# Kernel tuning notes

Hardware: AMD Instinct MI355X
Metric: run time of the kernel (lower is better)

The kernel has to match this reference:

```python
import jax, jax.numpy as jnp
import numpy as np

LN_EPS = 1e-6

def _log_g(x):
    return jnp.where(x >= 0, jnp.log(jax.nn.relu(x) + 0.5), -jax.nn.softplus(-x))

def setup_inputs() -> dict:
    key = jax.random.key(0)
    k1, k2 = jax.random.split(key)
    B, T, D = 8, 4096, 1024
    x = jax.random.normal(k1, (B, T, D), dtype=jnp.float32)
    W = jax.random.normal(k2, (D, 2 * D), dtype=jnp.float32) * (1.0 / np.sqrt(D))
    b = jnp.zeros((2 * D,), dtype=jnp.float32)
    gamma = jnp.ones((D,), dtype=jnp.float32)
    beta = jnp.zeros((D,), dtype=jnp.float32)
    return {"x": x, "W": W, "b": b, "gamma": gamma, "beta": beta}

def reference(x, W, b, gamma, beta):
    # projection: [B,T,D] @ [D,2D] -> [B,T,2D]
    projected = jnp.einsum('btd,de->bte', x, W) + b
    h_tilde, k = jnp.split(projected, 2, axis=-1)
    log_coeffs = -jax.nn.softplus(k)          # log(1-z)
    log_z = -jax.nn.softplus(-k)               # log(z)
    log_values = log_z + _log_g(h_tilde)
    # parallel scan in log space along time axis (-2)
    a_star = jnp.cumsum(log_coeffs, axis=-2)
    log_h0_plus_b_star = jax.lax.associative_scan(jnp.logaddexp, log_values - a_star, axis=-2)
    h = jnp.exp(a_star + log_h0_plus_b_star)
    # residual + LayerNorm (eps = flax nnx default 1e-6)
    y = x + h
    mu = jnp.mean(y, axis=-1, keepdims=True)
    var = jnp.mean(jnp.square(y - mu), axis=-1, keepdims=True)
    return (y - mu) * jax.lax.rsqrt(var + LN_EPS) * gamma + beta
```

## Files before the change

kernel.cpp:

```cpp
#include <hip/hip_runtime.h>
#include <hip/hip_bf16.h>

#define B_  8
#define T_  4096
#define D_  1024
#define M_  (B_*T_)
#define N_  (2*D_)
#define K_  D_
#define NC_ 32
#define C_  (T_/NC_)

typedef short bf16x8 __attribute__((ext_vector_type(8)));
typedef float f32x4  __attribute__((ext_vector_type(4)));

__device__ __forceinline__ unsigned short f2bf(float f) {
  union { float f; unsigned int u; } v; v.f = f;
  unsigned int r = (v.u + 0x7fffu + ((v.u >> 16) & 1u)) >> 16;
  return (unsigned short)r;
}

__device__ __forceinline__ float bf2f(unsigned short u) {
  union { unsigned int u; float f; } v; v.u = ((unsigned int)u) << 16; return v.f;
}

__device__ __forceinline__ float sigm(float x) {
  return 1.0f / (1.0f + __expf(-x));
}

__device__ __forceinline__ void async16(const void* g, void* l) {
  __builtin_amdgcn_global_load_lds((const __attribute__((address_space(1))) void*)g,
                                   (__attribute__((address_space(3))) void*)l,
                                   16, 0, 0);
}

__global__ void cast_x_kernel(const float* __restrict__ x, unsigned short* __restrict__ xb) {
  const long n4 = (long)M_ * K_ / 4;
  long i = (long)blockIdx.x * blockDim.x + threadIdx.x;
  const long stride = (long)gridDim.x * blockDim.x;
  for (; i < n4; i += stride) {
    float4 v = ((const float4*)x)[i];
    ushort4 o;
    o.x = f2bf(v.x); o.y = f2bf(v.y); o.z = f2bf(v.z); o.w = f2bf(v.w);
    ((ushort4*)xb)[i] = o;
  }
}

__global__ void cast_wt_kernel(const float* __restrict__ W, unsigned short* __restrict__ Wt) {
  __shared__ float tile[32][33];
  const int n0 = blockIdx.x * 32, k0 = blockIdx.y * 32;
  const int tx = threadIdx.x, ty = threadIdx.y;
  for (int i = 0; i < 32; i += 8)
    tile[ty + i][tx] = W[(size_t)(k0 + ty + i) * N_ + n0 + tx];
  __syncthreads();
  for (int i = 0; i < 32; i += 8)
    Wt[(size_t)(n0 + ty + i) * K_ + k0 + tx] = f2bf(tile[tx][ty + i]);
}

#define BM 256
#define BN 256
#define BK 64
#define NT (K_/BK)
#define LDSA(b) ((b)*32768)
#define LDSB(b) ((b)*32768 + 16384)

#define BARX()  __builtin_amdgcn_s_barrier()
#define LGKM0() asm volatile("s_waitcnt lgkmcnt(0)" ::: "memory")
#define SB0()   __builtin_amdgcn_sched_barrier(0)
#define VM8()   asm volatile("s_waitcnt vmcnt(8)" ::: "memory")
#define VM0()   asm volatile("s_waitcnt vmcnt(0)" ::: "memory")

#define STAGE_Bt(BUF, KOFF) do {                                                \
    _Pragma("unroll")                                                           \
    for (int r = 0; r < 4; ++r)                                                 \
      async16(aB + (KOFF) + r*64*K_, lds + LDSB(BUF) + w*512 + r*4096);         \
  } while (0)
#define STAGE_At(BUF, KOFF) do {                                                \
    _Pragma("unroll")                                                           \
    for (int r = 0; r < 4; ++r)                                                 \
      async16(aA + (KOFF) + r*64*K_, lds + LDSA(BUF) + w*512 + r*4096);         \
  } while (0)

#define RD_A(MBASE, BUF) do {                                                   \
    _Pragma("unroll")                                                           \
    for (int m = 0; m < 4; ++m) {                                               \
      af[m][0] = *(const bf16x8*)(lds + LDSA(BUF) + (rowA + (MBASE + m)*16)*64 + cc0); \
      af[m][1] = *(const bf16x8*)(lds + LDSA(BUF) + (rowA + (MBASE + m)*16)*64 + cc1); \
    } } while (0)
#define RD_B(NBASE, BUF) do {                                                   \
    _Pragma("unroll")                                                           \
    for (int n = 0; n < 2; ++n) {                                               \
      bfr[NBASE + n][0] = *(const bf16x8*)(lds + LDSB(BUF) + (rowB + (NBASE + n)*16)*64 + cc0); \
      bfr[NBASE + n][1] = *(const bf16x8*)(lds + LDSB(BUF) + (rowB + (NBASE + n)*16)*64 + cc1); \
    } } while (0)

#define MFMA_Q(MB, NB) do {                                                     \
    __builtin_amdgcn_s_setprio(1);                                              \
    _Pragma("unroll")                                                           \
    for (int m = 0; m < 4; ++m)                                                 \
      _Pragma("unroll")                                                         \
      for (int n = 0; n < 2; ++n) {                                             \
        acc[MB+m][NB+n] = __builtin_amdgcn_mfma_f32_16x16x32_bf16(af[m][0], bfr[NB+n][0], acc[MB+m][NB+n], 0, 0, 0); \
        acc[MB+m][NB+n] = __builtin_amdgcn_mfma_f32_16x16x32_bf16(af[m][1], bfr[NB+n][1], acc[MB+m][NB+n], 0, 0, 0); \
      }                                                                         \
    __builtin_amdgcn_s_setprio(0);                                              \
  } while (0)

#define TILE(BUF, DO_STAGE, KOFF, VMW) do {                                     \
                                                                        \
    RD_A(0, BUF); RD_B(0, BUF);                                                 \
    BARX(); LGKM0(); SB0();                                                     \
    MFMA_Q(0, 0);                                                               \
    BARX();                                                                     \
                                                                        \
    RD_B(2, BUF);                                                               \
    BARX(); LGKM0(); SB0();                                                     \
    MFMA_Q(0, 2);                                                               \
    BARX();                                                                     \
                                                                        \
    if (DO_STAGE) STAGE_Bt(BUF, KOFF);                                          \
    RD_A(4, BUF);                                                               \
    BARX(); LGKM0(); SB0();                                                     \
    MFMA_Q(4, 0);                                                               \
    BARX();                                                                     \
                                                                        \
    if (DO_STAGE) STAGE_At(BUF, KOFF);                                          \
    MFMA_Q(4, 2);                                                               \
    VMW;                                                                        \
    BARX();                                                                     \
  } while (0)

__global__ __launch_bounds__(512, 2) void gemm_kernel(
    const unsigned short* __restrict__ A,
    const unsigned short* __restrict__ Bt,
    const float* __restrict__ bias,
    unsigned short* __restrict__ Sout,
    unsigned short* __restrict__ Gout) {
  __shared__ unsigned short lds[65536];

  const int tid  = threadIdx.x;
  const int w    = tid >> 6;
  const int lane = tid & 63;
  const int wm   = w >> 2;
  const int wn   = w & 3;
  const int quad = lane >> 4, n15 = lane & 15;

  const int bid   = blockIdx.x;
  const int xcd   = bid & 7;
  const int j     = bid >> 3;
  const int n_idx = j & 7;
  const int m_idx = (j >> 3) * 8 + xcd;
  const int m0 = m_idx * BM, n0 = n_idx * BN;

  const int lr = lane >> 3, lg = lane & 7;
  const int sg8 = (lg ^ lr) * 8;
  const unsigned short* aA = A  + (size_t)(m0 + w*8 + lr) * K_ + sg8;
  const unsigned short* aB = Bt + (size_t)(n0 + w*8 + lr) * K_ + sg8;

  const int n7  = n15 & 7;
  const int cc0 = (quad ^ n7) * 8;
  const int cc1 = cc0 ^ 32;
  const int rowA = wm * 128 + n15;
  const int rowB = wn * 64  + n15;

  f32x4 acc[8][4];
  #pragma unroll
  for (int i = 0; i < 8; ++i)
    #pragma unroll
    for (int jj = 0; jj < 4; ++jj) acc[i][jj] = (f32x4){0.f, 0.f, 0.f, 0.f};

  bf16x8 af[4][2], bfr[4][2];

  STAGE_Bt(0, 0);  STAGE_At(0, 0);
  STAGE_Bt(1, 64); STAGE_At(1, 64);
  VM8();
  BARX();

  int koff = 128;
  #pragma unroll 1
  for (int it = 0; it < 7; ++it) {
    TILE(0, 1, koff,      VM8());
    TILE(1, 1, koff + 64, VM8());
    koff += 128;
  }
  TILE(0, 0, 0, VM0());
  TILE(1, 0, 0, ((void)0));

  const bool is_k = (n0 >= D_);
  unsigned short* __restrict__ dst = is_k ? Sout : Gout;
  const int d0 = is_k ? (n0 - D_) : n0;
  float bv[4];
  #pragma unroll
  for (int jj = 0; jj < 4; ++jj) bv[jj] = bias[n0 + wn*64 + jj*16 + n15];

  #pragma unroll
  for (int i = 0; i < 8; ++i) {
    #pragma unroll
    for (int jj = 0; jj < 4; ++jj) {
      const int col = wn*64 + jj*16 + n15;
      #pragma unroll
      for (int r = 0; r < 4; ++r) {
        const int row = wm*128 + i*16 + quad*4 + r;
        const float val = acc[i][jj][r] + bv[jj];
        const float o = is_k ? sigm(val)
                             : ((val >= 0.0f) ? (val + 0.5f) : sigm(val));
        const int slot = (col >> 3) ^ (row & 7);
        lds[row*256 + slot*8 + (col & 7)] = f2bf(o);
      }
    }
  }
  __syncthreads();
  const int trow = tid >> 5;
  const int cg   = tid & 31;
  #pragma unroll
  for (int rr = 0; rr < 16; ++rr) {
    const int row = rr*16 + trow;
    const uint4 v = *(const uint4*)(lds + row*256 + ((cg ^ (row & 7)) * 8));
    *(uint4*)(dst + (size_t)(m0 + row) * D_ + d0 + cg*8) = v;
  }
}

__global__ void chunk_agg_kernel(const unsigned short* __restrict__ S,
                                 const unsigned short* __restrict__ G,
                                 float* __restrict__ AggA, float* __restrict__ AggV) {
  const int d = blockIdx.x * 256 + threadIdx.x;
  const int c = blockIdx.y;
  const int b = blockIdx.z;
  size_t base = ((size_t)b * T_ + (size_t)c * C_) * D_ + d;
  float Aa = 1.0f, V = 0.0f;
  for (int t = 0; t < C_; ++t) {
    const float s = bf2f(S[base]);
    const float g = bf2f(G[base]);
    const float a = 1.0f - s;
    V = fmaf(a, V, s * g);
    Aa *= a;
    base += D_;
  }
  const int idx = (b * NC_ + c) * D_ + d;
  AggA[idx] = Aa;
  AggV[idx] = V;
}

__global__ void chunk_scan_kernel(const float* __restrict__ AggA, const float* __restrict__ AggV,
                                  float* __restrict__ H0) {
  const int d = blockIdx.x * 256 + threadIdx.x;
  const int b = blockIdx.y;
  float h = 0.0f;
  for (int c = 0; c < NC_; ++c) {
    const int idx = (b * NC_ + c) * D_ + d;
    H0[idx] = h;
    h = fmaf(AggA[idx], h, AggV[idx]);
  }
}

__global__ __launch_bounds__(1024, 1) void scan_ln_kernel(
    const unsigned short* __restrict__ S, const unsigned short* __restrict__ G,
    const float* __restrict__ x, const float* __restrict__ H0,
    const float* __restrict__ gamma, const float* __restrict__ beta,
    float* __restrict__ out) {
  __shared__ float yb[16 * 1024];
  const int d = threadIdx.x;
  const int c = blockIdx.x;
  const int b = blockIdx.y;
  const int wid = d >> 6, lane = d & 63;

  float h = H0[(b * NC_ + c) * D_ + d];
  float gam[16], bet[16];
  for (int j = 0; j < 16; ++j) { gam[j] = gamma[lane + 64 * j]; bet[j] = beta[lane + 64 * j]; }

  size_t base = ((size_t)b * T_ + (size_t)c * C_) * D_ + d;
  for (int batch = 0; batch < 8; ++batch) {
    for (int tt = 0; tt < 16; ++tt) {
      const size_t idx = base + (size_t)tt * D_;
      const float s = bf2f(S[idx]);
      const float g = bf2f(G[idx]);
      h = fmaf(s, g - h, h);
      yb[tt * 1024 + d] = x[idx] + h;
    }
    __syncthreads();
    {
      float sy = 0.0f, sq = 0.0f;
      float yv[16];
      for (int j = 0; j < 16; ++j) {
        const float v = yb[wid * 1024 + lane + 64 * j];
        yv[j] = v; sy += v; sq += v * v;
      }
      for (int o = 32; o > 0; o >>= 1) {
        sy += __shfl_down(sy, o);
        sq += __shfl_down(sq, o);
      }
      sy = __shfl(sy, 0); sq = __shfl(sq, 0);
      const float mu   = sy * (1.0f / D_);
      const float rstd = rsqrtf(sq * (1.0f / D_) - mu * mu + 1e-6f);
      const size_t obase = ((size_t)b * T_ + (size_t)c * C_ + (size_t)batch * 16 + wid) * D_;
      for (int j = 0; j < 16; ++j)
        out[obase + lane + 64 * j] = (yv[j] - mu) * rstd * gam[j] + bet[j];
    }
    __syncthreads();
    base += (size_t)16 * D_;
  }
}

extern "C" void kernel_launch(void* const* d_in, const int* in_sizes, int n_in,
                              void* d_out, int out_size, void* d_ws, size_t ws_size,
                              hipStream_t stream) {
  const float* x     = (const float*)d_in[0];
  const float* W     = (const float*)d_in[1];
  const float* bias  = (const float*)d_in[2];
  const float* gamma = (const float*)d_in[3];
  const float* beta  = (const float*)d_in[4];
  float* out = (float*)d_out;

  char* ws = (char*)d_ws;
  unsigned short* Wt = (unsigned short*)ws;  ws += (size_t)N_ * K_ * 2;
  unsigned short* Xb = (unsigned short*)ws;  ws += (size_t)M_ * K_ * 2;
  unsigned short* S  = (unsigned short*)ws;  ws += (size_t)M_ * D_ * 2;
  unsigned short* G  = (unsigned short*)ws;  ws += (size_t)M_ * D_ * 2;
  float* AggA = (float*)ws;                  ws += (size_t)B_ * NC_ * D_ * 4;
  float* AggV = (float*)ws;                  ws += (size_t)B_ * NC_ * D_ * 4;
  float* H0   = (float*)ws;                  ws += (size_t)B_ * NC_ * D_ * 4;

  cast_x_kernel<<<4096, 256, 0, stream>>>(x, Xb);
  cast_wt_kernel<<<dim3(N_ / 32, K_ / 32), dim3(32, 8), 0, stream>>>(W, Wt);
  gemm_kernel<<<1024, 512, 0, stream>>>(Xb, Wt, bias, S, G);
  chunk_agg_kernel<<<dim3(D_ / 256, NC_, B_), 256, 0, stream>>>(S, G, AggA, AggV);
  chunk_scan_kernel<<<dim3(D_ / 256, B_), 256, 0, stream>>>(AggA, AggV, H0);
  scan_ln_kernel<<<dim3(NC_, B_), 1024, 0, stream>>>(S, G, x, H0, gamma, beta, out);
}
```

Measured before the change: 477.1 us.

## Restructure GEMM mainloop to single-stage prefetch with one barrier per K-tile

Replaces the two-tile-ahead pipeline, which used four barrier/lgkmcnt phases per K-tile, with a scheme that prefetches only the next K-tile into the other LDS buffer. Each tile is one block of LDS reads followed by MFMAs, ending with a full vmcnt(0) wait and __syncthreads. B fragments are split into two register arrays so all B reads happen up front, and A is read in two halves. The aim is to cut barrier and waitcnt overhead inside the loop. The cost is less latency hiding for global loads (one tile ahead instead of two) plus extra register pressure from holding all B fragments at once.

New measurement: 475.6 us. No clear change (-0.3%).

```diff
diff --git a/kernel.cpp b/kernel.cpp
--- a/kernel.cpp
+++ b/kernel.cpp
@@ -59,14 +59,10 @@
 #define BM 256
 #define BN 256
 #define BK 64
-#define NT (K_/BK)
 #define LDSA(b) ((b)*32768)
 #define LDSB(b) ((b)*32768 + 16384)
 
-#define BARX()  __builtin_amdgcn_s_barrier()
-#define LGKM0() asm volatile("s_waitcnt lgkmcnt(0)" ::: "memory")
 #define SB0()   __builtin_amdgcn_sched_barrier(0)
-#define VM8()   asm volatile("s_waitcnt vmcnt(8)" ::: "memory")
 #define VM0()   asm volatile("s_waitcnt vmcnt(0)" ::: "memory")
 
 #define STAGE_Bt(BUF, KOFF) do {                                                \
@@ -80,53 +76,43 @@
       async16(aA + (KOFF) + r*64*K_, lds + LDSA(BUF) + w*512 + r*4096);         \
   } while (0)
 
-#define RD_A(MBASE, BUF) do {                                                   \
+#define RD_A8(MBASE, BUF) do {                                                  \
     _Pragma("unroll")                                                           \
     for (int m = 0; m < 4; ++m) {                                               \
-      af[m][0] = *(const bf16x8*)(lds + LDSA(BUF) + (rowA + (MBASE + m)*16)*64 + cc0); \
-      af[m][1] = *(const bf16x8*)(lds + LDSA(BUF) + (rowA + (MBASE + m)*16)*64 + cc1); \
+      afA[m][0] = *(const bf16x8*)(lds + LDSA(BUF) + (rowA + (MBASE + m)*16)*64 + cc0); \
+      afA[m][1] = *(const bf16x8*)(lds + LDSA(BUF) + (rowA + (MBASE + m)*16)*64 + cc1); \
     } } while (0)
-#define RD_B(NBASE, BUF) do {                                                   \
+#define RD_B4(ARR, NBASE, BUF) do {                                             \
     _Pragma("unroll")                                                           \
     for (int n = 0; n < 2; ++n) {                                               \
-      bfr[NBASE + n][0] = *(const bf16x8*)(lds + LDSB(BUF) + (rowB + (NBASE + n)*16)*64 + cc0); \
-      bfr[NBASE + n][1] = *(const bf16x8*)(lds + LDSB(BUF) + (rowB + (NBASE + n)*16)*64 + cc1); \
+      ARR[n][0] = *(const bf16x8*)(lds + LDSB(BUF) + (rowB + (NBASE + n)*16)*64 + cc0); \
+      ARR[n][1] = *(const bf16x8*)(lds + LDSB(BUF) + (rowB + (NBASE + n)*16)*64 + cc1); \
     } } while (0)
 
-#define MFMA_Q(MB, NB) do {                                                     \
+#define MQ(BARR, MB, NB) do {                                                   \
     __builtin_amdgcn_s_setprio(1);                                              \
     _Pragma("unroll")                                                           \
     for (int m = 0; m < 4; ++m)                                                 \
       _Pragma("unroll")                                                         \
       for (int n = 0; n < 2; ++n) {                                             \
-        acc[MB+m][NB+n] = __builtin_amdgcn_mfma_f32_16x16x32_bf16(af[m][0], bfr[NB+n][0], acc[MB+m][NB+n], 0, 0, 0); \
-        acc[MB+m][NB+n] = __builtin_amdgcn_mfma_f32_16x16x32_bf16(af[m][1], bfr[NB+n][1], acc[MB+m][NB+n], 0, 0, 0); \
+        acc[MB+m][NB+n] = __builtin_amdgcn_mfma_f32_16x16x32_bf16(afA[m][0], BARR[n][0], acc[MB+m][NB+n], 0, 0, 0); \
+        acc[MB+m][NB+n] = __builtin_amdgcn_mfma_f32_16x16x32_bf16(afA[m][1], BARR[n][1], acc[MB+m][NB+n], 0, 0, 0); \
       }                                                                         \
     __builtin_amdgcn_s_setprio(0);                                              \
   } while (0)
 
-#define TILE(BUF, DO_STAGE, KOFF, VMW) do {                                     \
-                                                                        \
-    RD_A(0, BUF); RD_B(0, BUF);                                                 \
-    BARX(); LGKM0(); SB0();                                                     \
-    MFMA_Q(0, 0);                                                               \
-    BARX();                                                                     \
-                                                                        \
-    RD_B(2, BUF);                                                               \
-    BARX(); LGKM0(); SB0();                                                     \
-    MFMA_Q(0, 2);                                                               \
-    BARX();                                                                     \
-                                                                        \
-    if (DO_STAGE) STAGE_Bt(BUF, KOFF);                                          \
-    RD_A(4, BUF);                                                               \
-    BARX(); LGKM0(); SB0();                                                     \
-    MFMA_Q(4, 0);                                                               \
-    BARX();                                                                     \
-                                                                        \
-    if (DO_STAGE) STAGE_At(BUF, KOFF);                                          \
-    MFMA_Q(4, 2);                                                               \
-    VMW;                                                                        \
-    BARX();                                                                     \
+#define TILE_V2(BR, BW, DO_STAGE, KOFF) do {                                    \
+    RD_A8(0, BR);                                     \
+    RD_B4(bfrA, 0, BR);                               \
+    RD_B4(bfrB, 2, BR);                               \
+    if (DO_STAGE) { STAGE_Bt(BW, KOFF); STAGE_At(BW, KOFF); SB0(); }            \
+    MQ(bfrA, 0, 0);                                            \
+    MQ(bfrB, 0, 2);                                            \
+    RD_A8(4, BR);                                    \
+    MQ(bfrB, 4, 2);                                            \
+    MQ(bfrA, 4, 0);                                            \
+    VM0();                                                                      \
+    __syncthreads();                                                            \
   } while (0)
 
 __global__ __launch_bounds__(512, 2) void gemm_kernel(
@@ -168,22 +154,21 @@
     #pragma unroll
     for (int jj = 0; jj < 4; ++jj) acc[i][jj] = (f32x4){0.f, 0.f, 0.f, 0.f};
 
-  bf16x8 af[4][2], bfr[4][2];
+  bf16x8 afA[4][2], bfrA[2][2], bfrB[2][2];
 
   STAGE_Bt(0, 0);  STAGE_At(0, 0);
-  STAGE_Bt(1, 64); STAGE_At(1, 64);
-  VM8();
-  BARX();
-
-  int koff = 128;
+  VM0();
+  __syncthreads();
+
+  int koff = 64;
   #pragma unroll 1
   for (int it = 0; it < 7; ++it) {
-    TILE(0, 1, koff,      VM8());
-    TILE(1, 1, koff + 64, VM8());
+    TILE_V2(0, 1, 1, koff);
+    TILE_V2(1, 0, 1, koff + 64);
     koff += 128;
   }
-  TILE(0, 0, 0, VM0());
-  TILE(1, 0, 0, ((void)0));
+  TILE_V2(0, 1, 1, koff);
+  TILE_V2(1, 0, 0, 0);
 
   const bool is_k = (n0 >= D_);
   unsigned short* __restrict__ dst = is_k ? Sout : Gout;
```
